# Kernel tuning notes

Hardware: AMD Instinct MI355X
Metric: run time of the kernel (lower is better)

## Reference

```python
import math
import jax, jax.numpy as jnp
import numpy as np

H = 8      # head_count
M = 9      # box window over key positions (odd)
N = 3      # box window over key heads (odd)


def _box(x, w, axis):
    """Sliding box-sum of width w with SAME padding ((w-1)//2 each side).
    Mathematically identical to F.conv1d with an all-ones kernel of size w."""
    p = (w - 1) // 2
    pad = [(0, 0)] * x.ndim
    pad[axis] = (p, p)
    xp = jnp.pad(x, pad)
    c = jnp.cumsum(xp, axis=axis)
    pad2 = [(0, 0)] * x.ndim
    pad2[axis] = (1, 0)
    c = jnp.pad(c, pad2)
    n = x.shape[axis]
    hi = jax.lax.slice_in_dim(c, w, w + n, axis=axis)
    lo = jax.lax.slice_in_dim(c, 0, n, axis=axis)
    return hi - lo


def _scatter_idx(b, h, q, k, m, n):
    """Flat destination indices reproducing torch masked_scatter_ semantics:
    source elements are consumed in flat order and written to masked slots."""
    hw = (n - 1) // 2
    pw = (m - 1) // 2
    hi = np.arange(h)
    head_mask = np.abs(hi[:, None] - hi[None, :]) <= hw          # (h, h)
    qi = np.arange(q)
    ki = np.arange(k)
    pos_mask = np.abs(qi[:, None] - ki[None, :]) <= pw           # (q, k)
    mw = head_mask[:, None, :, None] | pos_mask[None, :, None, :]  # (h,q,h,k)
    flat = np.flatnonzero(mw.reshape(-1)).astype(np.int64)
    per = h * q * h * k
    idx = (np.arange(b, dtype=np.int64)[:, None] * per + flat[None, :]).reshape(-1)
    return idx


def setup_inputs() -> dict:
    key = jax.random.key(0)
    ks = jax.random.split(key, 12)
    B, S, D = 2, 512, 512
    sc = 1.0 / math.sqrt(D)
    inp = {
        "key_in": jax.random.normal(ks[0], (B, S, D), jnp.float32),
        "value_in": jax.random.normal(ks[1], (B, S, D), jnp.float32),
        "query_in": jax.random.normal(ks[2], (B, S, D), jnp.float32),
        "mask": jax.random.bernoulli(ks[3], 0.05, (B, S, S)),
        "Wq": jax.random.normal(ks[4], (D, D), jnp.float32) * sc,
        "bq": jnp.zeros((D,), jnp.float32),
        "Wk": jax.random.normal(ks[5], (D, D), jnp.float32) * sc,
        "bk": jnp.zeros((D,), jnp.float32),
        "Wv": jax.random.normal(ks[6], (D, D), jnp.float32) * sc,
        "bv": jnp.zeros((D,), jnp.float32),
        "Wo": jax.random.normal(ks[7], (D, D), jnp.float32) * sc,
        "bo": jnp.zeros((D,), jnp.float32),
    }
    return inp


def reference(key_in, value_in, query_in, mask, Wq, bq, Wk, bk, Wv, bv, Wo, bo):
    B, S, D = key_in.shape
    h = H
    dh = D // h

    def proj(x, W, b):
        # nn.Linear then shape(): (B, S, D) -> (B, h, S, dh)
        return (x @ W.T + b).reshape(B, S, h, dh).transpose(0, 2, 1, 3)

    q = proj(query_in, Wq, bq) / math.sqrt(dh)
    k = proj(key_in, Wk, bk)
    v = proj(value_in, Wv, bv)

    qf = q.reshape(B, h * S, dh)
    kf = k.reshape(B, h * S, dh)
    vf = v.reshape(B, h * S, dh)

    # cross-head scores: (B, H*Sq, H*Sk) viewed as (B, qh, q, kh, k)
    scores = jnp.einsum("bid,bjd->bij", qf, kf).astype(jnp.float32)
    scores = scores.reshape(B, h, S, h, S)
    scores = jnp.where(mask[:, None, :, None, :], jnp.float32(-1e18), scores)

    # convolSoftmax: exp then box-normalize over a (N kh) x (M kpos) window
    e = jnp.exp(scores)                       # (B, qh, q, kh, k)
    denom = _box(_box(e, M, axis=4), N, axis=3)
    attn = (e / denom).astype(query_in.dtype)

    # masked_scatter_: attn elements in flat order -> masked slots of zeros
    idx = jnp.asarray(_scatter_idx(B, h, S, S, M, N))
    flat = attn.reshape(-1)
    attn_masked = jnp.zeros_like(flat).at[idx].set(flat[: idx.shape[0]])
    attn_masked = attn_masked.reshape(B, h * S, h * S)

    ctx = jnp.einsum("bij,bjd->bid", attn_masked, vf)   # (B, H*S, dh)
    # faithful 'unshape' on the 3D tensor: transpose(1,2) then view(B,-1,H*dh)
    ctx = jnp.transpose(ctx, (0, 2, 1)).reshape(B, S, h * dh)
    out = ctx @ Wo.T + bo

    top_attn = attn[:, 0, :, 0, :]
    return out, top_attn
```

## Files before the change

kernel.cpp:

```cpp
#include <hip/hip_runtime.h>
#include <math.h>


__global__ void zero_kernel(int* __restrict__ flags)
{
    if (threadIdx.x < 2) flags[threadIdx.x] = 0;
}

__global__ __launch_bounds__(256) void detect_kernel(const unsigned int* __restrict__ mask_words,
                                                     int* __restrict__ flags)
{
    __shared__ int sh[2];
    if (threadIdx.x == 0) { sh[0] = 0; sh[1] = 0; }
    __syncthreads();
    int bad_int = 0, bad_f32 = 0;
    int base = blockIdx.x * 2048;
    for (int t = threadIdx.x; t < 2048; t += 256) {
        unsigned w = mask_words[base + t];
        if (w > 1u) bad_int = 1;
        if (w != 0u && w != 0x3F800000u) bad_f32 = 1;
    }
    if (bad_int) atomicOr(&sh[0], 1);
    if (bad_f32) atomicOr(&sh[1], 1);
    __syncthreads();
    if (threadIdx.x == 0) {
        if (sh[0]) atomicOr(&flags[0], 1);
        if (sh[1]) atomicOr(&flags[1], 1);
    }
}

__global__ __launch_bounds__(256) void proj3_kernel(const float* __restrict__ Xq, const float* __restrict__ Xk,
                                                    const float* __restrict__ Xv,
                                                    const float* __restrict__ Wq, const float* __restrict__ Wk,
                                                    const float* __restrict__ Wv,
                                                    const float* __restrict__ bq, const float* __restrict__ bk,
                                                    const float* __restrict__ bv,
                                                    float* __restrict__ dq, float* __restrict__ dk,
                                                    float* __restrict__ dv)
{
    const float* X; const float* W; const float* bias; float* dst; float scale;
    if (blockIdx.z == 0)      { X = Xq; W = Wq; bias = bq; dst = dq; scale = 0.125f; }
    else if (blockIdx.z == 1) { X = Xk; W = Wk; bias = bk; dst = dk; scale = 1.0f; }
    else                      { X = Xv; W = Wv; bias = bv; dst = dv; scale = 1.0f; }

    __shared__ float As[64][17], Bs[64][17];
    int tx = threadIdx.x & 15, ty = threadIdx.x >> 4;
    int r0 = blockIdx.y * 64, o0 = blockIdx.x * 64;
    float acc[4][4] = {};
    for (int k0 = 0; k0 < 512; k0 += 16) {
#pragma unroll
        for (int l = 0; l < 4; ++l) {
            int idx = threadIdx.x + l * 256;
            int r = idx >> 4, c = idx & 15;
            As[r][c] = X[(size_t)(r0 + r) * 512 + k0 + c];
            Bs[r][c] = W[(size_t)(o0 + r) * 512 + k0 + c];
        }
        __syncthreads();
#pragma unroll
        for (int kk = 0; kk < 16; ++kk) {
            float a[4], bb[4];
#pragma unroll
            for (int i = 0; i < 4; ++i) a[i] = As[ty * 4 + i][kk];
#pragma unroll
            for (int j = 0; j < 4; ++j) bb[j] = Bs[tx * 4 + j][kk];
#pragma unroll
            for (int i = 0; i < 4; ++i)
#pragma unroll
                for (int j = 0; j < 4; ++j) acc[i][j] = fmaf(a[i], bb[j], acc[i][j]);
        }
        __syncthreads();
    }
#pragma unroll
    for (int i = 0; i < 4; ++i) {
        int r = r0 + ty * 4 + i;
        int b = r >> 9, s = r & 511;
#pragma unroll
        for (int j = 0; j < 4; ++j) {
            int o = o0 + tx * 4 + j;
            float v = (acc[i][j] + bias[o]) * scale;
            dst[(((size_t)b * 8 + (o >> 6)) * 512 + s) * 64 + (o & 63)] = v;
        }
    }
}

__global__ __launch_bounds__(256) void scores_kernel(const float* __restrict__ qh, const float* __restrict__ kh,
                                                     float* __restrict__ scores)
{
    __shared__ float As[64][65], Bs[64][65];
    int r0 = blockIdx.y * 64, c0 = blockIdx.x * 64;
    int b1 = (r0 >= 3072);
    const float* Ab = qh + (b1 ? (size_t)1024 * 64 : 0);
    const float* Bb = kh + (b1 ? (size_t)4096 * 64 : 0);
#pragma unroll
    for (int l = 0; l < 16; ++l) {
        int idx = threadIdx.x + l * 256;
        int r = idx >> 6, c = idx & 63;
        As[r][c] = Ab[(size_t)(r0 + r) * 64 + c];
        Bs[r][c] = Bb[(size_t)(c0 + r) * 64 + c];
    }
    __syncthreads();
    int tx = threadIdx.x & 15, ty = threadIdx.x >> 4;
    float acc[4][4] = {};
#pragma unroll 8
    for (int kk = 0; kk < 64; ++kk) {
        float a[4], bb[4];
#pragma unroll
        for (int i = 0; i < 4; ++i) a[i] = As[ty * 4 + i][kk];
#pragma unroll
        for (int j = 0; j < 4; ++j) bb[j] = Bs[tx * 4 + j][kk];
#pragma unroll
        for (int i = 0; i < 4; ++i)
#pragma unroll
            for (int j = 0; j < 4; ++j) acc[i][j] = fmaf(a[i], bb[j], acc[i][j]);
    }
#pragma unroll
    for (int i = 0; i < 4; ++i)
#pragma unroll
        for (int j = 0; j < 4; ++j)
            scores[(size_t)(r0 + ty * 4 + i) * 4096 + (c0 + tx * 4 + j)] = acc[i][j];
}

#define EIDX(h, k) (((h) * 544) + (k) + ((k) >> 4))
__global__ __launch_bounds__(256) void attn_kernel(float* __restrict__ scores, const void* __restrict__ mask,
                                                   const int* __restrict__ flags, float* __restrict__ top_out)
{
    __shared__ float e[8 * 544];
    int row = blockIdx.x;
    int b = (row >= 3072);
    int hq = b ? 0 : (row >> 9);
    int q  = b ? (row - 3072) : (row & 511);
    float* rp = scores + (size_t)row * 4096;
    int mode = (!flags[0]) ? 0 : ((!flags[1]) ? 2 : 1);
    int t = threadIdx.x;
    int hk = t >> 5;
    int k0 = (t & 31) << 4;
    int j0 = (hk << 9) + k0;
    size_t mrow = ((size_t)b * 512 + q) * 512 + k0;

    float sv[16];
    {
        const float4* p4 = reinterpret_cast<const float4*>(rp + j0);
#pragma unroll
        for (int l = 0; l < 4; ++l) {
            float4 v = p4[l];
            sv[l * 4 + 0] = v.x; sv[l * 4 + 1] = v.y; sv[l * 4 + 2] = v.z; sv[l * 4 + 3] = v.w;
        }
    }
    bool mv[16];
    if (mode == 0) {
        const int4* mp = reinterpret_cast<const int4*>((const int*)mask + mrow);
#pragma unroll
        for (int l = 0; l < 4; ++l) {
            int4 w = mp[l];
            mv[l * 4 + 0] = w.x != 0; mv[l * 4 + 1] = w.y != 0;
            mv[l * 4 + 2] = w.z != 0; mv[l * 4 + 3] = w.w != 0;
        }
    } else if (mode == 2) {
        const float4* mp = reinterpret_cast<const float4*>((const float*)mask + mrow);
#pragma unroll
        for (int l = 0; l < 4; ++l) {
            float4 w = mp[l];
            mv[l * 4 + 0] = w.x != 0.0f; mv[l * 4 + 1] = w.y != 0.0f;
            mv[l * 4 + 2] = w.z != 0.0f; mv[l * 4 + 3] = w.w != 0.0f;
        }
    } else {
        uint4 w = *reinterpret_cast<const uint4*>((const unsigned char*)mask + mrow);
        unsigned int ws[4] = {w.x, w.y, w.z, w.w};
#pragma unroll
        for (int i = 0; i < 16; ++i) mv[i] = ((ws[i >> 2] >> ((i & 3) * 8)) & 0xFFu) != 0u;
    }

    float ev[16];
#pragma unroll
    for (int i = 0; i < 16; ++i) ev[i] = mv[i] ? 0.0f : __expf(sv[i]);
#pragma unroll
    for (int i = 0; i < 16; ++i) e[EIDX(hk, k0 + i)] = ev[i];
    __syncthreads();

    float d[16] = {};
#pragma unroll
    for (int dr = -1; dr <= 1; ++dr) {
        int hh = hk + dr;
        if (hh < 0 || hh > 7) continue;
        float w24[24];
#pragma unroll
        for (int p = 0; p < 24; ++p) {
            int kk = k0 + p - 4;
            w24[p] = (kk >= 0 && kk < 512) ? e[EIDX(hh, kk)] : 0.0f;
        }
        float pr[25];
        pr[0] = 0.0f;
#pragma unroll
        for (int p = 0; p < 24; ++p) pr[p + 1] = pr[p] + w24[p];
#pragma unroll
        for (int i = 0; i < 16; ++i) d[i] += pr[i + 9] - pr[i];
    }

    float av[16];
#pragma unroll
    for (int i = 0; i < 16; ++i) av[i] = ev[i] / d[i];

    {
        float4* p4 = reinterpret_cast<float4*>(rp + j0);
#pragma unroll
        for (int l = 0; l < 4; ++l) {
            float4 v;
            v.x = av[l * 4 + 0]; v.y = av[l * 4 + 1]; v.z = av[l * 4 + 2]; v.w = av[l * 4 + 3];
            p4[l] = v;
        }
    }
    if (hq == 0 && hk == 0) {
        float4* p4 = reinterpret_cast<float4*>(top_out + mrow);
#pragma unroll
        for (int l = 0; l < 4; ++l) {
            float4 v;
            v.x = av[l * 4 + 0]; v.y = av[l * 4 + 1]; v.z = av[l * 4 + 2]; v.w = av[l * 4 + 3];
            p4[l] = v;
        }
    }
}

__global__ __launch_bounds__(256) void ctx_kernel(const float* __restrict__ attn_src, const float* __restrict__ vh,
                                                  float* __restrict__ ctxT, float* __restrict__ part1,
                                                  float* __restrict__ part2)
{
    __shared__ float As[2][32][34];
    __shared__ float Vs[2][32][64];
    __shared__ int rowOff[32];

    int tid = threadIdx.x;
    int tx = tid & 15;
    int ty = tid >> 4;
    int q0 = blockIdx.x * 32;
    int hq = blockIdx.y;
    int bz = blockIdx.z;
    int b = bz / 3;
    int ks = bz % 3;

    int hkLo = (hq - 1 < 0) ? 0 : hq - 1;
    int hkHi = (hq + 1 > 7) ? 7 : hq + 1;
    int nband = hkHi - hkLo + 1;
    float* dst = (ks == 0) ? ctxT : ((ks == 1) ? part1 : part2);

    if (ks >= nband) {
#pragma unroll
        for (int i = 0; i < 2; ++i) {
            int q = q0 + ty * 2 + i;
#pragma unroll
            for (int j = 0; j < 4; ++j)
                dst[((size_t)b * 512 + (tx * 4 + j) * 8 + hq) * 512 + q] = 0.0f;
        }
        return;
    }

    if (tid < 32) {
        int q = q0 + tid;
        int A = (hq > 0) ? (551816 + (hq - 1) * 809372) : 0;
        int nHP = (hq == 0 || hq == 7) ? 2 : 3;
        int s1 = (q >= 5) ? 10 : (4 * q - (q * (q - 1)) / 2);
        int s2 = (q <= 508) ? 0 : ((q - 508) * (q - 507)) / 2;
        int pref = 9 * q - s1 - s2;
        int rb = A + nHP * 512 * q + (8 - nHP) * pref;
        int lo = (q - 4 < 0) ? 0 : q - 4;
        int hi = (q + 4 > 511) ? 511 : q + 4;
        rowOff[tid] = b * 5959864 + rb + hkLo * (hi - lo + 1);
    }
    __syncthreads();

    int ac = tid & 31;
    int aq = tid >> 5;
    int ro[4];
#pragma unroll
    for (int l = 0; l < 4; ++l) ro[l] = rowOff[aq + 8 * l];
    int vr = tid >> 4, vc = (tid & 15) * 4;
    int hk = hkLo + ks;
    int bandAdd = ks << 9;
    const float* vb = vh + (((size_t)b * 8 + hk) * 512) * 64;

    float pa[4]; float4 pv[2];
#define CTX_LOAD(S) { \
        int kk0_ = (S) << 5; \
        _Pragma("unroll") \
        for (int l = 0; l < 4; ++l) pa[l] = attn_src[ro[l] + bandAdd + kk0_ + ac]; \
        _Pragma("unroll") \
        for (int l = 0; l < 2; ++l) \
            pv[l] = *reinterpret_cast<const float4*>(vb + (size_t)(kk0_ + vr + 16 * l) * 64 + vc); \
    }
#define CTX_WRITE(BUF) { \
        _Pragma("unroll") \
        for (int l = 0; l < 4; ++l) As[BUF][ac][aq + 8 * l] = pa[l]; \
        _Pragma("unroll") \
        for (int l = 0; l < 2; ++l) \
            *reinterpret_cast<float4*>(&Vs[BUF][vr + 16 * l][vc]) = pv[l]; \
    }

    CTX_LOAD(0);
    CTX_WRITE(0);
    CTX_LOAD(1);

    float acc[2][4] = {};
    int ty2 = ty * 2;
    int cur = 0;
    for (int s = 0; s < 16; ++s) {
        __syncthreads();
#pragma unroll
        for (int kk = 0; kk < 32; ++kk) {
            float2 a = *reinterpret_cast<const float2*>(&As[cur][kk][ty2]);
            float4 v = *reinterpret_cast<const float4*>(&Vs[cur][kk][tx * 4]);
            acc[0][0] = fmaf(a.x, v.x, acc[0][0]); acc[0][1] = fmaf(a.x, v.y, acc[0][1]);
            acc[0][2] = fmaf(a.x, v.z, acc[0][2]); acc[0][3] = fmaf(a.x, v.w, acc[0][3]);
            acc[1][0] = fmaf(a.y, v.x, acc[1][0]); acc[1][1] = fmaf(a.y, v.y, acc[1][1]);
            acc[1][2] = fmaf(a.y, v.z, acc[1][2]); acc[1][3] = fmaf(a.y, v.w, acc[1][3]);
        }
        if (s + 1 < 16) {
            CTX_WRITE(cur ^ 1);
            if (s + 2 < 16) CTX_LOAD(s + 2);
        }
        cur ^= 1;
    }

    if (ks == 0) {
#pragma unroll
        for (int i = 0; i < 2; ++i) {
            int q = q0 + ty2 + i;
            int lo = (q - 4 < 0) ? 0 : q - 4;
            int hi = (q + 4 > 511) ? 511 : q + 4;
            int cnt = hi - lo + 1;
            int cOff = rowOff[ty2 + i] - hkLo * cnt;
            int t = 0;
            for (int hh = 0; hh < 8; ++hh) {
                if (hh >= hkLo && hh <= hkHi) { t += 512; continue; }
                const float* vbase = vh + (((size_t)b * 8 + hh) * 512) * 64 + tx * 4;
                for (int k = lo; k <= hi; ++k) {
                    float a = attn_src[cOff + t]; ++t;
                    const float4 v = *reinterpret_cast<const float4*>(vbase + (size_t)k * 64);
                    acc[i][0] = fmaf(a, v.x, acc[i][0]);
                    acc[i][1] = fmaf(a, v.y, acc[i][1]);
                    acc[i][2] = fmaf(a, v.z, acc[i][2]);
                    acc[i][3] = fmaf(a, v.w, acc[i][3]);
                }
            }
        }
    }

#pragma unroll
    for (int i = 0; i < 2; ++i) {
        int q = q0 + ty2 + i;
#pragma unroll
        for (int j = 0; j < 4; ++j)
            dst[((size_t)b * 512 + (tx * 4 + j) * 8 + hq) * 512 + q] = acc[i][j];
    }
}

__global__ __launch_bounds__(256) void out_kernel(const float* __restrict__ ctxT, const float* __restrict__ part1,
                                                  const float* __restrict__ part2,
                                                  const float* __restrict__ Wo,
                                                  const float* __restrict__ bo, float* __restrict__ out)
{
    __shared__ float As[64][17], Bs[64][17];
    int b = blockIdx.z;
    int r0 = blockIdx.y * 64, o0 = blockIdx.x * 64;
    const float* A = ctxT + (size_t)b * 512 * 512;
    const float* P1 = part1 + (size_t)b * 512 * 512;
    const float* P2 = part2 + (size_t)b * 512 * 512;
    int tx = threadIdx.x & 15, ty = threadIdx.x >> 4;
    float acc[4][4] = {};
    for (int k0 = 0; k0 < 512; k0 += 16) {
#pragma unroll
        for (int l = 0; l < 4; ++l) {
            int idx = threadIdx.x + l * 256;
            int r = idx >> 4, c = idx & 15;
            size_t ai = (size_t)(r0 + r) * 512 + k0 + c;
            As[r][c] = A[ai] + P1[ai] + P2[ai];
            Bs[r][c] = Wo[(size_t)(o0 + r) * 512 + k0 + c];
        }
        __syncthreads();
#pragma unroll
        for (int kk = 0; kk < 16; ++kk) {
            float a[4], bb[4];
#pragma unroll
            for (int i = 0; i < 4; ++i) a[i] = As[ty * 4 + i][kk];
#pragma unroll
            for (int j = 0; j < 4; ++j) bb[j] = Bs[tx * 4 + j][kk];
#pragma unroll
            for (int i = 0; i < 4; ++i)
#pragma unroll
                for (int j = 0; j < 4; ++j) acc[i][j] = fmaf(a[i], bb[j], acc[i][j]);
        }
        __syncthreads();
    }
#pragma unroll
    for (int i = 0; i < 4; ++i) {
        int r = r0 + ty * 4 + i;
#pragma unroll
        for (int j = 0; j < 4; ++j) {
            int o = o0 + tx * 4 + j;
            out[((size_t)b * 512 + r) * 512 + o] = acc[i][j] + bo[o];
        }
    }
}

extern "C" void kernel_launch(void* const* d_in, const int* in_sizes, int n_in,
                              void* d_out, int out_size, void* d_ws, size_t ws_size,
                              hipStream_t stream)
{
    const float* key_in   = (const float*)d_in[0];
    const float* value_in = (const float*)d_in[1];
    const float* query_in = (const float*)d_in[2];
    const void*  mask     = d_in[3];
    const float* Wq = (const float*)d_in[4];
    const float* bq = (const float*)d_in[5];
    const float* Wk = (const float*)d_in[6];
    const float* bk = (const float*)d_in[7];
    const float* Wv = (const float*)d_in[8];
    const float* bv = (const float*)d_in[9];
    const float* Wo = (const float*)d_in[10];
    const float* bo = (const float*)d_in[11];

    float* ws = (float*)d_ws;
    float* qh = ws;
    float* kh = qh + 524288;
    float* vh = kh + 524288;
    float* scores = vh + 524288;
    float* ctxT = scores + 14680064;
    int* flags = (int*)(ctxT + 524288);

    float* out = (float*)d_out;
    float* top = out + 524288;

    zero_kernel<<<1, 64, 0, stream>>>(flags);
    detect_kernel<<<64, 256, 0, stream>>>((const unsigned int*)mask, flags);
    proj3_kernel<<<dim3(8, 16, 3), 256, 0, stream>>>(query_in, key_in, value_in,
                                                     Wq, Wk, Wv, bq, bk, bv, qh, kh, vh);
    scores_kernel<<<dim3(64, 56), 256, 0, stream>>>(qh, kh, scores);
    attn_kernel<<<3584, 256, 0, stream>>>(scores, mask, flags, top);
    ctx_kernel<<<dim3(16, 8, 6), 256, 0, stream>>>(scores, vh, ctxT, qh, kh);
    out_kernel<<<dim3(8, 8, 2), 256, 0, stream>>>(ctxT, qh, kh, Wo, bo, out);
}
```

Measured before the change: 298.2 us.

## Double-buffer and vectorize GEMM tiles in projection, scores and output kernels

The projection and output GEMMs now use a k-major transposed shared-memory layout with a 32-wide K step, float4 global loads, and register-prefetched double buffering, so there is one barrier per step instead of two. The scores kernel gets the same transposed layout and float4 loads. The inner loops read float4 from shared memory, which cuts LDS instruction count. The transposed scalar stores into shared memory may cause bank conflicts, and the prefetch registers add register pressure.

```diff
diff --git a/kernel.cpp b/kernel.cpp
--- a/kernel.cpp
+++ b/kernel.cpp
@@ -43,33 +43,58 @@
     else if (blockIdx.z == 1) { X = Xk; W = Wk; bias = bk; dst = dk; scale = 1.0f; }
     else                      { X = Xv; W = Wv; bias = bv; dst = dv; scale = 1.0f; }
 
-    __shared__ float As[64][17], Bs[64][17];
-    int tx = threadIdx.x & 15, ty = threadIdx.x >> 4;
+    __shared__ float As[2][32][68], Bs[2][32][68];
+    int tid = threadIdx.x;
+    int tx = tid & 15, ty = tid >> 4;
     int r0 = blockIdx.y * 64, o0 = blockIdx.x * 64;
+    int sr = tid >> 2, sc = (tid & 3) * 8;
+    const float* Xp = X + (size_t)(r0 + sr) * 512 + sc;
+    const float* Wp = W + (size_t)(o0 + sr) * 512 + sc;
+
+    float4 pa0, pa1, pb0, pb1;
+#define P3_LOAD(K0) { \
+        pa0 = *reinterpret_cast<const float4*>(Xp + (K0)); \
+        pa1 = *reinterpret_cast<const float4*>(Xp + (K0) + 4); \
+        pb0 = *reinterpret_cast<const float4*>(Wp + (K0)); \
+        pb1 = *reinterpret_cast<const float4*>(Wp + (K0) + 4); }
+#define P3_WRITE(BUF) { \
+        As[BUF][sc + 0][sr] = pa0.x; As[BUF][sc + 1][sr] = pa0.y; \
+        As[BUF][sc + 2][sr] = pa0.z; As[BUF][sc + 3][sr] = pa0.w; \
+        As[BUF][sc + 4][sr] = pa1.x; As[BUF][sc + 5][sr] = pa1.y; \
+        As[BUF][sc + 6][sr] = pa1.z; As[BUF][sc + 7][sr] = pa1.w; \
+        Bs[BUF][sc + 0][sr] = pb0.x; Bs[BUF][sc + 1][sr] = pb0.y; \
+        Bs[BUF][sc + 2][sr] = pb0.z; Bs[BUF][sc + 3][sr] = pb0.w; \
+        Bs[BUF][sc + 4][sr] = pb1.x; Bs[BUF][sc + 5][sr] = pb1.y; \
+        Bs[BUF][sc + 6][sr] = pb1.z; Bs[BUF][sc + 7][sr] = pb1.w; }
+
+    P3_LOAD(0);
+    P3_WRITE(0);
+    P3_LOAD(32);
+
     float acc[4][4] = {};
-    for (int k0 = 0; k0 < 512; k0 += 16) {
-#pragma unroll
-        for (int l = 0; l < 4; ++l) {
-            int idx = threadIdx.x + l * 256;
-            int r = idx >> 4, c = idx & 15;
-            As[r][c] = X[(size_t)(r0 + r) * 512 + k0 + c];
-            Bs[r][c] = W[(size_t)(o0 + r) * 512 + k0 + c];
-        }
+    int cur = 0;
+    for (int s = 0; s < 16; ++s) {
         __syncthreads();
 #pragma unroll
-        for (int kk = 0; kk < 16; ++kk) {
-            float a[4], bb[4];
-#pragma unroll
-            for (int i = 0; i < 4; ++i) a[i] = As[ty * 4 + i][kk];
-#pragma unroll
-            for (int j = 0; j < 4; ++j) bb[j] = Bs[tx * 4 + j][kk];
-#pragma unroll
-            for (int i = 0; i < 4; ++i)
-#pragma unroll
-                for (int j = 0; j < 4; ++j) acc[i][j] = fmaf(a[i], bb[j], acc[i][j]);
-        }
-        __syncthreads();
-    }
+        for (int kk = 0; kk < 32; ++kk) {
+            float4 a = *reinterpret_cast<const float4*>(&As[cur][kk][ty * 4]);
+            float4 bv = *reinterpret_cast<const float4*>(&Bs[cur][kk][tx * 4]);
+            acc[0][0] = fmaf(a.x, bv.x, acc[0][0]); acc[0][1] = fmaf(a.x, bv.y, acc[0][1]);
+            acc[0][2] = fmaf(a.x, bv.z, acc[0][2]); acc[0][3] = fmaf(a.x, bv.w, acc[0][3]);
+            acc[1][0] = fmaf(a.y, bv.x, acc[1][0]); acc[1][1] = fmaf(a.y, bv.y, acc[1][1]);
+            acc[1][2] = fmaf(a.y, bv.z, acc[1][2]); acc[1][3] = fmaf(a.y, bv.w, acc[1][3]);
+            acc[2][0] = fmaf(a.z, bv.x, acc[2][0]); acc[2][1] = fmaf(a.z, bv.y, acc[2][1]);
+            acc[2][2] = fmaf(a.z, bv.z, acc[2][2]); acc[2][3] = fmaf(a.z, bv.w, acc[2][3]);
+            acc[3][0] = fmaf(a.w, bv.x, acc[3][0]); acc[3][1] = fmaf(a.w, bv.y, acc[3][1]);
+            acc[3][2] = fmaf(a.w, bv.z, acc[3][2]); acc[3][3] = fmaf(a.w, bv.w, acc[3][3]);
+        }
+        if (s + 1 < 16) {
+            P3_WRITE(cur ^ 1);
+            if (s + 2 < 16) P3_LOAD((s + 2) * 32);
+        }
+        cur ^= 1;
+    }
+
 #pragma unroll
     for (int i = 0; i < 4; ++i) {
         int r = r0 + ty * 4 + i;
@@ -86,32 +111,41 @@
 __global__ __launch_bounds__(256) void scores_kernel(const float* __restrict__ qh, const float* __restrict__ kh,
                                                      float* __restrict__ scores)
 {
-    __shared__ float As[64][65], Bs[64][65];
+    __shared__ float As[64][68], Bs[64][68];
+    int tid = threadIdx.x;
     int r0 = blockIdx.y * 64, c0 = blockIdx.x * 64;
     int b1 = (r0 >= 3072);
     const float* Ab = qh + (b1 ? (size_t)1024 * 64 : 0);
     const float* Bb = kh + (b1 ? (size_t)4096 * 64 : 0);
-#pragma unroll
-    for (int l = 0; l < 16; ++l) {
-        int idx = threadIdx.x + l * 256;
-        int r = idx >> 6, c = idx & 63;
-        As[r][c] = Ab[(size_t)(r0 + r) * 64 + c];
-        Bs[r][c] = Bb[(size_t)(c0 + r) * 64 + c];
+    int sr = tid >> 2, sc = (tid & 3) * 16;
+    {
+        const float* Ap = Ab + (size_t)(r0 + sr) * 64 + sc;
+        const float* Bp = Bb + (size_t)(c0 + sr) * 64 + sc;
+#pragma unroll
+        for (int l = 0; l < 4; ++l) {
+            float4 a = *reinterpret_cast<const float4*>(Ap + l * 4);
+            float4 b = *reinterpret_cast<const float4*>(Bp + l * 4);
+            As[sc + l * 4 + 0][sr] = a.x; As[sc + l * 4 + 1][sr] = a.y;
+            As[sc + l * 4 + 2][sr] = a.z; As[sc + l * 4 + 3][sr] = a.w;
+            Bs[sc + l * 4 + 0][sr] = b.x; Bs[sc + l * 4 + 1][sr] = b.y;
+            Bs[sc + l * 4 + 2][sr] = b.z; Bs[sc + l * 4 + 3][sr] = b.w;
+        }
     }
     __syncthreads();
-    int tx = threadIdx.x & 15, ty = threadIdx.x >> 4;
+    int tx = tid & 15, ty = tid >> 4;
     float acc[4][4] = {};
 #pragma unroll 8
     for (int kk = 0; kk < 64; ++kk) {
-        float a[4], bb[4];
-#pragma unroll
-        for (int i = 0; i < 4; ++i) a[i] = As[ty * 4 + i][kk];
-#pragma unroll
-        for (int j = 0; j < 4; ++j) bb[j] = Bs[tx * 4 + j][kk];
-#pragma unroll
-        for (int i = 0; i < 4; ++i)
-#pragma unroll
-            for (int j = 0; j < 4; ++j) acc[i][j] = fmaf(a[i], bb[j], acc[i][j]);
+        float4 a = *reinterpret_cast<const float4*>(&As[kk][ty * 4]);
+        float4 bv = *reinterpret_cast<const float4*>(&Bs[kk][tx * 4]);
+        acc[0][0] = fmaf(a.x, bv.x, acc[0][0]); acc[0][1] = fmaf(a.x, bv.y, acc[0][1]);
+        acc[0][2] = fmaf(a.x, bv.z, acc[0][2]); acc[0][3] = fmaf(a.x, bv.w, acc[0][3]);
+        acc[1][0] = fmaf(a.y, bv.x, acc[1][0]); acc[1][1] = fmaf(a.y, bv.y, acc[1][1]);
+        acc[1][2] = fmaf(a.y, bv.z, acc[1][2]); acc[1][3] = fmaf(a.y, bv.w, acc[1][3]);
+        acc[2][0] = fmaf(a.z, bv.x, acc[2][0]); acc[2][1] = fmaf(a.z, bv.y, acc[2][1]);
+        acc[2][2] = fmaf(a.z, bv.z, acc[2][2]); acc[2][3] = fmaf(a.z, bv.w, acc[2][3]);
+        acc[3][0] = fmaf(a.w, bv.x, acc[3][0]); acc[3][1] = fmaf(a.w, bv.y, acc[3][1]);
+        acc[3][2] = fmaf(a.w, bv.z, acc[3][2]); acc[3][3] = fmaf(a.w, bv.w, acc[3][3]);
     }
 #pragma unroll
     for (int i = 0; i < 4; ++i)
@@ -357,38 +391,60 @@
                                                   const float* __restrict__ Wo,
                                                   const float* __restrict__ bo, float* __restrict__ out)
 {
-    __shared__ float As[64][17], Bs[64][17];
+    __shared__ float As[2][32][68], Bs[2][32][68];
+    int tid = threadIdx.x;
     int b = blockIdx.z;
     int r0 = blockIdx.y * 64, o0 = blockIdx.x * 64;
-    const float* A = ctxT + (size_t)b * 512 * 512;
-    const float* P1 = part1 + (size_t)b * 512 * 512;
-    const float* P2 = part2 + (size_t)b * 512 * 512;
-    int tx = threadIdx.x & 15, ty = threadIdx.x >> 4;
+    int tx = tid & 15, ty = tid >> 4;
+    int sr = tid >> 2, sc = (tid & 3) * 8;
+    const float* Ap = ctxT + (size_t)b * 262144 + (size_t)(r0 + sr) * 512 + sc;
+    const float* P1p = part1 + (size_t)b * 262144 + (size_t)(r0 + sr) * 512 + sc;
+    const float* P2p = part2 + (size_t)b * 262144 + (size_t)(r0 + sr) * 512 + sc;
+    const float* Wp = Wo + (size_t)(o0 + sr) * 512 + sc;
+
+    float4 pa0, pa1, pb0, pb1;
+#define OUT_LOAD(K0) { \
+        float4 a0 = *reinterpret_cast<const float4*>(Ap + (K0)); \
+        float4 a1 = *reinterpret_cast<const float4*>(Ap + (K0) + 4); \
+        float4 q0v = *reinterpret_cast<const float4*>(P1p + (K0)); \
+        float4 q1v = *reinterpret_cast<const float4*>(P1p + (K0) + 4); \
+        float4 r0v = *reinterpret_cast<const float4*>(P2p + (K0)); \
+        float4 r1v = *reinterpret_cast<const float4*>(P2p + (K0) + 4); \
+        pa0.x = a0.x + q0v.x + r0v.x; pa0.y = a0.y + q0v.y + r0v.y; \
+        pa0.z = a0.z + q0v.z + r0v.z; pa0.w = a0.w + q0v.w + r0v.w; \
+        pa1.x = a1.x + q1v.x + r1v.x; pa1.y = a1.y + q1v.y + r1v.y; \
+        pa1.z = a1.z + q1v.z + r1v.z; pa1.w = a1.w + q1v.w + r1v.w; \
+        pb0 = *reinterpret_cast<const float4*>(Wp + (K0)); \
+        pb1 = *reinterpret_cast<const float4*>(Wp + (K0) + 4); }
+
+    OUT_LOAD(0);
+    P3_WRITE(0);
+    OUT_LOAD(32);
+
     float acc[4][4] = {};
-    for (int k0 = 0; k0 < 512; k0 += 16) {
-#pragma unroll
-        for (int l = 0; l < 4; ++l) {
-            int idx = threadIdx.x + l * 256;
-            int r = idx >> 4, c = idx & 15;
-            size_t ai = (size_t)(r0 + r) * 512 + k0 + c;
-            As[r][c] = A[ai] + P1[ai] + P2[ai];
-            Bs[r][c] = Wo[(size_t)(o0 + r) * 512 + k0 + c];
-        }
+    int cur = 0;
+    for (int s = 0; s < 16; ++s) {
         __syncthreads();
 #pragma unroll
-        for (int kk = 0; kk < 16; ++kk) {
-            float a[4], bb[4];
-#pragma unroll
-            for (int i = 0; i < 4; ++i) a[i] = As[ty * 4 + i][kk];
-#pragma unroll
-            for (int j = 0; j < 4; ++j) bb[j] = Bs[tx * 4 + j][kk];
-#pragma unroll
-            for (int i = 0; i < 4; ++i)
-#pragma unroll
-                for (int j = 0; j < 4; ++j) acc[i][j] = fmaf(a[i], bb[j], acc[i][j]);
-        }
-        __syncthreads();
-    }
+        for (int kk = 0; kk < 32; ++kk) {
+            float4 a = *reinterpret_cast<const float4*>(&As[cur][kk][ty * 4]);
+            float4 bv = *reinterpret_cast<const float4*>(&Bs[cur][kk][tx * 4]);
+            acc[0][0] = fmaf(a.x, bv.x, acc[0][0]); acc[0][1] = fmaf(a.x, bv.y, acc[0][1]);
+            acc[0][2] = fmaf(a.x, bv.z, acc[0][2]); acc[0][3] = fmaf(a.x, bv.w, acc[0][3]);
+            acc[1][0] = fmaf(a.y, bv.x, acc[1][0]); acc[1][1] = fmaf(a.y, bv.y, acc[1][1]);
+            acc[1][2] = fmaf(a.y, bv.z, acc[1][2]); acc[1][3] = fmaf(a.y, bv.w, acc[1][3]);
+            acc[2][0] = fmaf(a.z, bv.x, acc[2][0]); acc[2][1] = fmaf(a.z, bv.y, acc[2][1]);
+            acc[2][2] = fmaf(a.z, bv.z, acc[2][2]); acc[2][3] = fmaf(a.z, bv.w, acc[2][3]);
+            acc[3][0] = fmaf(a.w, bv.x, acc[3][0]); acc[3][1] = fmaf(a.w, bv.y, acc[3][1]);
+            acc[3][2] = fmaf(a.w, bv.z, acc[3][2]); acc[3][3] = fmaf(a.w, bv.w, acc[3][3]);
+        }
+        if (s + 1 < 16) {
+            P3_WRITE(cur ^ 1);
+            if (s + 2 < 16) OUT_LOAD((s + 2) * 32);
+        }
+        cur ^= 1;
+    }
+
 #pragma unroll
     for (int i = 0; i < 4; ++i) {
         int r = r0 + ty * 4 + i;
```

Result: faster. 268.3 us (-10.0%).
